# Performance work log

Hardware: AMD Instinct MI355X
Metric: run time of the kernel (lower is better)

Reference implementation:

```python
import jax, jax.numpy as jnp
import numpy as np
from jax import lax

B, C, P = 8, 32, 256      # batch, channels, patch side
KB = 2                    # buf_region = kernel_size - stride = 3 - 1
R_MASK = 1                # output_bypassing: last-column patch, r = small_padding = 1


def setup_inputs() -> dict:
    key = jax.random.key(0)
    ks = jax.random.split(key, 5)
    x = jax.random.normal(ks[0], (B, C, P, P), jnp.float32)
    # right-halo stored by the left-neighbor patch (store_right -> last 2 cols)
    rbuf = jax.random.normal(ks[1], (B, C, P, KB), jnp.float32)
    # bottom-halo stored by the top-neighbor patch AFTER its hcat (width P+2)
    bbuf = jax.random.normal(ks[2], (B, C, KB, P + KB), jnp.float32)
    W = jax.random.normal(ks[3], (C, C, 3, 3), jnp.float32) * 0.05
    bias = jax.random.normal(ks[4], (C,), jnp.float32) * 0.05
    return {"x": x, "rbuf": rbuf, "bbuf": bbuf, "W": W, "bias": bias}


def reference(x, rbuf, bbuf, W, bias):
    # output_bypassing: zero the rightmost R_MASK columns (image right edge)
    x = x.at[:, :, :, -R_MASK:].set(0.0)
    # hcat: prepend right-halo from left neighbor -> [B,C,P,P+2]
    x = jnp.concatenate([rbuf, x], axis=-1)
    # vcat: prepend bottom-halo from top neighbor -> [B,C,P+2,P+2]
    x = jnp.concatenate([bbuf, x], axis=-2)
    # (store_bot side effect omitted: pure function returns conv output only)
    out = lax.conv_general_dilated(
        x, W, window_strides=(1, 1), padding='VALID',
        dimension_numbers=('NCHW', 'OIHW', 'NCHW'))  # -> [B,C,P,P]
    return out + bias[None, :, None, None]
```

## Files before the change

kernel.cpp:

```cpp
#include <hip/hip_runtime.h>
#include <cstdint>


constexpr int B  = 8;
constexpr int C  = 32;
constexpr int P  = 256;
constexpr int KB = 2;
constexpr int TILE = 16;
constexpr int RS = 20;
constexpr int PL = 364;
constexpr int XSZ = 16 * PL;

typedef short bf16x8 __attribute__((ext_vector_type(8)));
typedef float f32x4  __attribute__((ext_vector_type(4)));
union Frag { uint32_t u[4]; bf16x8 v; };

static __device__ __forceinline__ uint32_t pk_bf16(float lo, float hi) {
    uint32_t a  = __builtin_bit_cast(uint32_t, lo);
    uint32_t b2 = __builtin_bit_cast(uint32_t, hi);
    a  += 0x7FFFu + ((a  >> 16) & 1u);
    b2 += 0x7FFFu + ((b2 >> 16) & 1u);
    return (a >> 16) | (b2 & 0xFFFF0000u);
}

struct Staged {
    float4 ilo[4], ihi[4];
    float  tlo[4], thi[4];
    float  llo[4], lhi[4];
};

__global__ __launch_bounds__(256, 2) void conv_mfma(
    const float* __restrict__ x,
    const float* __restrict__ rbuf,
    const float* __restrict__ bbuf,
    const float* __restrict__ W,
    const float* __restrict__ bias,
    float* __restrict__ out)
{
    const int tid  = threadIdx.x;
    const int lane = tid & 63;
    const int w    = tid >> 6;
    const int q    = lane >> 4;
    const int n16  = lane & 15;

    const int blk = blockIdx.x;
    const int tx = blk & 15, ty = (blk >> 4) & 15, b0 = blk >> 8;
    const int x0 = tx * TILE, y0 = ty * TILE;

    __shared__ uint32_t Xs[2 * XSZ];
    __shared__ uint32_t Ws[9 * 512];

    #pragma unroll
    for (int k = 0; k < 18; ++k) {
        const int u  = tid + k * 256;
        const int m  = u & 15;
        const int oc = (u >> 4) & 31;
        const int t  = u >> 9;
        const float lo = W[(oc * C + 2 * m) * 9 + t];
        const float hi = W[(oc * C + 2 * m + 1) * 9 + t];
        Ws[t * 512 + oc * 16 + m] = pk_bf16(lo, hi);
    }

    const int irow  = lane >> 2;
    const int icol4 = (lane & 3) * 4;
    const bool zc   = (x0 == P - TILE) && ((lane & 3) == 3);

    const int t_r = lane >= 18 ? 1 : 0;
    const int t_c = lane - 18 * t_r;
    int t_sel = 0, t_off = 0; bool t_zero = false;
    {
        const int rg = y0 + t_r, cg = x0 + t_c;
        if (rg < KB)      { t_sel = 2; t_off = rg * (P + KB) + cg; }
        else if (cg < KB) { t_sel = 1; t_off = (rg - KB) * KB + cg; }
        else              { t_sel = 0; t_off = (rg - KB) * P + (cg - KB);
                            t_zero = (cg == P + KB - 1); }
    }
    const int l_r = lane >> 1;
    const int l_c = lane & 1;
    int l_sel = 0, l_off = 0;
    {
        const int rg = y0 + KB + l_r, cg = x0 + l_c;
        if (cg < KB) { l_sel = 1; l_off = (rg - KB) * KB + cg; }
        else         { l_sel = 0; l_off = (rg - KB) * P + (cg - KB); }
    }

    auto stage_load = [&](int bt, Staged& S) {
        const float* xb = x    + (size_t)bt * C * P * P;
        const float* rb = rbuf + (size_t)bt * C * P * KB;
        const float* bb = bbuf + (size_t)bt * C * KB * (P + KB);
        const float* basep[3] = { xb, rb, bb };
        const int    psz[3]   = { P * P, P * KB, KB * (P + KB) };
        #pragma unroll
        for (int k2 = 0; k2 < 4; ++k2) {
            const int m = 4 * k2 + w;
            const float* pi = xb + (2 * m) * (P * P) + (y0 + irow) * P + x0 + icol4;
            S.ilo[k2] = *(const float4*)pi;
            S.ihi[k2] = *(const float4*)(pi + P * P);
            if (lane < 36) {
                const float* pt = basep[t_sel] + (size_t)(2 * m) * psz[t_sel] + t_off;
                S.tlo[k2] = t_zero ? 0.f : pt[0];
                S.thi[k2] = t_zero ? 0.f : pt[psz[t_sel]];
            }
            if (lane < 32) {
                const float* pl = basep[l_sel] + (size_t)(2 * m) * psz[l_sel] + l_off;
                S.llo[k2] = pl[0];
                S.lhi[k2] = pl[psz[l_sel]];
            }
        }
    };

    auto stage_store = [&](uint32_t* Xb, Staged& S) {
        #pragma unroll
        for (int k2 = 0; k2 < 4; ++k2) {
            const int m = 4 * k2 + w;
            float4 lo = S.ilo[k2], hi = S.ihi[k2];
            if (zc) { lo.w = 0.f; hi.w = 0.f; }
            uint32_t* dst = Xb + m * PL + (irow + KB) * RS + (icol4 + KB);
            dst[0] = pk_bf16(lo.x, hi.x);
            dst[1] = pk_bf16(lo.y, hi.y);
            dst[2] = pk_bf16(lo.z, hi.z);
            dst[3] = pk_bf16(lo.w, hi.w);
            if (lane < 36) Xb[m * PL + t_r * RS + t_c]         = pk_bf16(S.tlo[k2], S.thi[k2]);
            if (lane < 32) Xb[m * PL + (l_r + KB) * RS + l_c]  = pk_bf16(S.llo[k2], S.lhi[k2]);
        }
    };

    Staged S;
    stage_load(b0, S);
    stage_store(Xs, S);
    __syncthreads();

    Frag Bf[9][2];
    #pragma unroll
    for (int t = 0; t < 9; ++t)
        #pragma unroll
        for (int oh = 0; oh < 2; ++oh) {
            const uint32_t* src = &Ws[t * 512 + (oh * 16 + n16) * 16 + q * 4];
            Bf[t][oh].u[0] = src[0]; Bf[t][oh].u[1] = src[1];
            Bf[t][oh].u[2] = src[2]; Bf[t][oh].u[3] = src[3];
        }
    const float bv0 = bias[n16];
    const float bv1 = bias[16 + n16];

    for (int t = 0; t < 4; ++t) {
        const uint32_t* Xc = Xs + (t & 1) * XSZ;
        const int bt = b0 + 2 * t;

        if (t < 3) stage_load(b0 + 2 * (t + 1), S);

        f32x4 acc[4][2];
        #pragma unroll
        for (int rr = 0; rr < 4; ++rr)
            #pragma unroll
            for (int oh = 0; oh < 2; ++oh)
                #pragma unroll
                for (int e = 0; e < 4; ++e) acc[rr][oh][e] = 0.f;

        #pragma unroll
        for (int dr = 0; dr < 6; ++dr) {
            Frag A[3];
            const uint32_t* ap = Xc + (4 * q) * PL + (4 * w + dr) * RS + n16;
            #pragma unroll
            for (int kx = 0; kx < 3; ++kx)
                #pragma unroll
                for (int p = 0; p < 4; ++p)
                    A[kx].u[p] = ap[p * PL + kx];
            #pragma unroll
            for (int ky = 0; ky < 3; ++ky) {
                const int rr = dr - ky;
                if (rr >= 0 && rr < 4) {
                    #pragma unroll
                    for (int kx = 0; kx < 3; ++kx) {
                        acc[rr][0] = __builtin_amdgcn_mfma_f32_16x16x32_bf16(
                                         A[kx].v, Bf[ky * 3 + kx][0].v, acc[rr][0], 0, 0, 0);
                        acc[rr][1] = __builtin_amdgcn_mfma_f32_16x16x32_bf16(
                                         A[kx].v, Bf[ky * 3 + kx][1].v, acc[rr][1], 0, 0, 0);
                    }
                }
            }
        }

        #pragma unroll
        for (int oh = 0; oh < 2; ++oh) {
            const int oc = oh * 16 + n16;
            const float bv = oh ? bv1 : bv0;
            #pragma unroll
            for (int rr = 0; rr < 4; ++rr) {
                float4 v;
                v.x = acc[rr][oh][0] + bv;
                v.y = acc[rr][oh][1] + bv;
                v.z = acc[rr][oh][2] + bv;
                v.w = acc[rr][oh][3] + bv;
                *(float4*)&out[((size_t)(bt * C + oc) * P + (y0 + 4 * w + rr)) * P + x0 + 4 * q] = v;
            }
        }

        if (t < 3) stage_store(Xs + ((t + 1) & 1) * XSZ, S);
        __syncthreads();
    }
}

extern "C" void kernel_launch(void* const* d_in, const int* in_sizes, int n_in,
                              void* d_out, int out_size, void* d_ws, size_t ws_size,
                              hipStream_t stream) {
    const float* x    = (const float*)d_in[0];
    const float* rbuf = (const float*)d_in[1];
    const float* bbuf = (const float*)d_in[2];
    const float* W    = (const float*)d_in[3];
    const float* bias = (const float*)d_in[4];
    float* out = (float*)d_out;

    conv_mfma<<<512, 256, 0, stream>>>(x, rbuf, bbuf, W, bias, out);
}
```

Baseline: 149.6 us.

## Replace batch-looped double-buffered blocks with one batch per block and shared LDS

Each block now handles a single batch image instead of looping over four batches with a double-buffered input tile. The grid grows from 512 to 2048 blocks. Weights and the input tile now reuse one shared LDS array, with an extra barrier between them, and the launch-bounds occupancy hint rises from 2 to 4 blocks. The goal is more parallelism and occupancy to hide memory latency rather than relying on software pipelining. The cost is that weight loading and bf16 packing are now repeated per block, four times as often overall.

Result: slower. 192.8 us (+28.8%).

```diff
diff --git a/kernel.cpp b/kernel.cpp
--- a/kernel.cpp
+++ b/kernel.cpp
@@ -23,13 +23,7 @@
     return (a >> 16) | (b2 & 0xFFFF0000u);
 }
 
-struct Staged {
-    float4 ilo[4], ihi[4];
-    float  tlo[4], thi[4];
-    float  llo[4], lhi[4];
-};
-
-__global__ __launch_bounds__(256, 2) void conv_mfma(
+__global__ __launch_bounds__(256, 4) void conv_mfma(
     const float* __restrict__ x,
     const float* __restrict__ rbuf,
     const float* __restrict__ bbuf,
@@ -44,11 +38,10 @@
     const int n16  = lane & 15;
 
     const int blk = blockIdx.x;
-    const int tx = blk & 15, ty = (blk >> 4) & 15, b0 = blk >> 8;
+    const int tx = blk & 15, ty = (blk >> 4) & 15, b = blk >> 8;
     const int x0 = tx * TILE, y0 = ty * TILE;
 
-    __shared__ uint32_t Xs[2 * XSZ];
-    __shared__ uint32_t Ws[9 * 512];
+    __shared__ uint32_t Xs[XSZ];
 
     #pragma unroll
     for (int k = 0; k < 18; ++k) {
@@ -58,7 +51,7 @@
         const int t  = u >> 9;
         const float lo = W[(oc * C + 2 * m) * 9 + t];
         const float hi = W[(oc * C + 2 * m + 1) * 9 + t];
-        Ws[t * 512 + oc * 16 + m] = pk_bf16(lo, hi);
+        Xs[t * 512 + oc * 16 + m] = pk_bf16(lo, hi);
     }
 
     const int irow  = lane >> 2;
@@ -84,50 +77,34 @@
         else         { l_sel = 0; l_off = (rg - KB) * P + (cg - KB); }
     }
 
-    auto stage_load = [&](int bt, Staged& S) {
-        const float* xb = x    + (size_t)bt * C * P * P;
-        const float* rb = rbuf + (size_t)bt * C * P * KB;
-        const float* bb = bbuf + (size_t)bt * C * KB * (P + KB);
-        const float* basep[3] = { xb, rb, bb };
-        const int    psz[3]   = { P * P, P * KB, KB * (P + KB) };
-        #pragma unroll
-        for (int k2 = 0; k2 < 4; ++k2) {
-            const int m = 4 * k2 + w;
-            const float* pi = xb + (2 * m) * (P * P) + (y0 + irow) * P + x0 + icol4;
-            S.ilo[k2] = *(const float4*)pi;
-            S.ihi[k2] = *(const float4*)(pi + P * P);
-            if (lane < 36) {
-                const float* pt = basep[t_sel] + (size_t)(2 * m) * psz[t_sel] + t_off;
-                S.tlo[k2] = t_zero ? 0.f : pt[0];
-                S.thi[k2] = t_zero ? 0.f : pt[psz[t_sel]];
-            }
-            if (lane < 32) {
-                const float* pl = basep[l_sel] + (size_t)(2 * m) * psz[l_sel] + l_off;
-                S.llo[k2] = pl[0];
-                S.lhi[k2] = pl[psz[l_sel]];
-            }
+    const float* xb = x    + (size_t)b * C * P * P;
+    const float* rb = rbuf + (size_t)b * C * P * KB;
+    const float* bb = bbuf + (size_t)b * C * KB * (P + KB);
+    const float* basep[3] = { xb, rb, bb };
+    const int    psz[3]   = { P * P, P * KB, KB * (P + KB) };
+
+    uint32_t ipk[4][4], tpk[4], lpk[4];
+    #pragma unroll
+    for (int k2 = 0; k2 < 4; ++k2) {
+        const int m = 4 * k2 + w;
+        const float* pi = xb + (2 * m) * (P * P) + (y0 + irow) * P + x0 + icol4;
+        float4 lo = *(const float4*)pi;
+        float4 hi = *(const float4*)(pi + P * P);
+        if (zc) { lo.w = 0.f; hi.w = 0.f; }
+        ipk[k2][0] = pk_bf16(lo.x, hi.x);
+        ipk[k2][1] = pk_bf16(lo.y, hi.y);
+        ipk[k2][2] = pk_bf16(lo.z, hi.z);
+        ipk[k2][3] = pk_bf16(lo.w, hi.w);
+        if (lane < 36) {
+            const float* pt = basep[t_sel] + (size_t)(2 * m) * psz[t_sel] + t_off;
+            tpk[k2] = t_zero ? 0u : pk_bf16(pt[0], pt[psz[t_sel]]);
         }
-    };
+        if (lane < 32) {
+            const float* pl = basep[l_sel] + (size_t)(2 * m) * psz[l_sel] + l_off;
+            lpk[k2] = pk_bf16(pl[0], pl[psz[l_sel]]);
+        }
+    }
 
-    auto stage_store = [&](uint32_t* Xb, Staged& S) {
-        #pragma unroll
-        for (int k2 = 0; k2 < 4; ++k2) {
-            const int m = 4 * k2 + w;
-            float4 lo = S.ilo[k2], hi = S.ihi[k2];
-            if (zc) { lo.w = 0.f; hi.w = 0.f; }
-            uint32_t* dst = Xb + m * PL + (irow + KB) * RS + (icol4 + KB);
-            dst[0] = pk_bf16(lo.x, hi.x);
-            dst[1] = pk_bf16(lo.y, hi.y);
-            dst[2] = pk_bf16(lo.z, hi.z);
-            dst[3] = pk_bf16(lo.w, hi.w);
-            if (lane < 36) Xb[m * PL + t_r * RS + t_c]         = pk_bf16(S.tlo[k2], S.thi[k2]);
-            if (lane < 32) Xb[m * PL + (l_r + KB) * RS + l_c]  = pk_bf16(S.llo[k2], S.lhi[k2]);
-        }
-    };
-
-    Staged S;
-    stage_load(b0, S);
-    stage_store(Xs, S);
     __syncthreads();
 
     Frag Bf[9][2];
@@ -135,68 +112,73 @@
     for (int t = 0; t < 9; ++t)
         #pragma unroll
         for (int oh = 0; oh < 2; ++oh) {
-            const uint32_t* src = &Ws[t * 512 + (oh * 16 + n16) * 16 + q * 4];
+            const uint32_t* src = &Xs[t * 512 + (oh * 16 + n16) * 16 + q * 4];
             Bf[t][oh].u[0] = src[0]; Bf[t][oh].u[1] = src[1];
             Bf[t][oh].u[2] = src[2]; Bf[t][oh].u[3] = src[3];
         }
     const float bv0 = bias[n16];
     const float bv1 = bias[16 + n16];
 
-    for (int t = 0; t < 4; ++t) {
-        const uint32_t* Xc = Xs + (t & 1) * XSZ;
-        const int bt = b0 + 2 * t;
+    __syncthreads();
 
-        if (t < 3) stage_load(b0 + 2 * (t + 1), S);
+    #pragma unroll
+    for (int k2 = 0; k2 < 4; ++k2) {
+        const int m = 4 * k2 + w;
+        uint32_t* dst = Xs + m * PL + (irow + KB) * RS + (icol4 + KB);
+        dst[0] = ipk[k2][0];
+        dst[1] = ipk[k2][1];
+        dst[2] = ipk[k2][2];
+        dst[3] = ipk[k2][3];
+        if (lane < 36) Xs[m * PL + t_r * RS + t_c]        = tpk[k2];
+        if (lane < 32) Xs[m * PL + (l_r + KB) * RS + l_c] = lpk[k2];
+    }
+    __syncthreads();
 
-        f32x4 acc[4][2];
+    f32x4 acc[4][2];
+    #pragma unroll
+    for (int rr = 0; rr < 4; ++rr)
         #pragma unroll
-        for (int rr = 0; rr < 4; ++rr)
+        for (int oh = 0; oh < 2; ++oh)
             #pragma unroll
-            for (int oh = 0; oh < 2; ++oh)
+            for (int e = 0; e < 4; ++e) acc[rr][oh][e] = 0.f;
+
+    #pragma unroll
+    for (int dr = 0; dr < 6; ++dr) {
+        Frag A[3];
+        const uint32_t* ap = Xs + (4 * q) * PL + (4 * w + dr) * RS + n16;
+        #pragma unroll
+        for (int kx = 0; kx < 3; ++kx)
+            #pragma unroll
+            for (int p = 0; p < 4; ++p)
+                A[kx].u[p] = ap[p * PL + kx];
+        #pragma unroll
+        for (int ky = 0; ky < 3; ++ky) {
+            const int rr = dr - ky;
+            if (rr >= 0 && rr < 4) {
                 #pragma unroll
-                for (int e = 0; e < 4; ++e) acc[rr][oh][e] = 0.f;
-
-        #pragma unroll
-        for (int dr = 0; dr < 6; ++dr) {
-            Frag A[3];
-            const uint32_t* ap = Xc + (4 * q) * PL + (4 * w + dr) * RS + n16;
-            #pragma unroll
-            for (int kx = 0; kx < 3; ++kx)
-                #pragma unroll
-                for (int p = 0; p < 4; ++p)
-                    A[kx].u[p] = ap[p * PL + kx];
-            #pragma unroll
-            for (int ky = 0; ky < 3; ++ky) {
-                const int rr = dr - ky;
-                if (rr >= 0 && rr < 4) {
-                    #pragma unroll
-                    for (int kx = 0; kx < 3; ++kx) {
-                        acc[rr][0] = __builtin_amdgcn_mfma_f32_16x16x32_bf16(
-                                         A[kx].v, Bf[ky * 3 + kx][0].v, acc[rr][0], 0, 0, 0);
-                        acc[rr][1] = __builtin_amdgcn_mfma_f32_16x16x32_bf16(
-                                         A[kx].v, Bf[ky * 3 + kx][1].v, acc[rr][1], 0, 0, 0);
-                    }
+                for (int kx = 0; kx < 3; ++kx) {
+                    acc[rr][0] = __builtin_amdgcn_mfma_f32_16x16x32_bf16(
+                                     A[kx].v, Bf[ky * 3 + kx][0].v, acc[rr][0], 0, 0, 0);
+                    acc[rr][1] = __builtin_amdgcn_mfma_f32_16x16x32_bf16(
+                                     A[kx].v, Bf[ky * 3 + kx][1].v, acc[rr][1], 0, 0, 0);
                 }
             }
         }
+    }
 
+    #pragma unroll
+    for (int oh = 0; oh < 2; ++oh) {
+        const int oc = oh * 16 + n16;
+        const float bv = oh ? bv1 : bv0;
         #pragma unroll
-        for (int oh = 0; oh < 2; ++oh) {
-            const int oc = oh * 16 + n16;
-            const float bv = oh ? bv1 : bv0;
-            #pragma unroll
-            for (int rr = 0; rr < 4; ++rr) {
-                float4 v;
-                v.x = acc[rr][oh][0] + bv;
-                v.y = acc[rr][oh][1] + bv;
-                v.z = acc[rr][oh][2] + bv;
-                v.w = acc[rr][oh][3] + bv;
-                *(float4*)&out[((size_t)(bt * C + oc) * P + (y0 + 4 * w + rr)) * P + x0 + 4 * q] = v;
-            }
+        for (int rr = 0; rr < 4; ++rr) {
+            float4 v;
+            v.x = acc[rr][oh][0] + bv;
+            v.y = acc[rr][oh][1] + bv;
+            v.z = acc[rr][oh][2] + bv;
+            v.w = acc[rr][oh][3] + bv;
+            *(float4*)&out[((size_t)(b * C + oc) * P + (y0 + 4 * w + rr)) * P + x0 + 4 * q] = v;
         }
-
-        if (t < 3) stage_store(Xs + ((t + 1) & 1) * XSZ, S);
-        __syncthreads();
     }
 }
 
@@ -210,5 +192,5 @@
     const float* bias = (const float*)d_in[4];
     float* out = (float*)d_out;
 
-    conv_mfma<<<512, 256, 0, stream>>>(x, rbuf, bbuf, W, bias, out);
+    conv_mfma<<<2048, 256, 0, stream>>>(x, rbuf, bbuf, W, bias, out);
 }
```
